# Kernel optimization log

Measured on AMD Instinct MI355X. Metric: run time of the kernel, lower is better.

The kernel has to match this reference:

```python
import jax, jax.numpy as jnp
import numpy as np

HIDDEN = 512
NUM_HEAD = 8
HEAD_DIM = HIDDEN // NUM_HEAD


def setup_inputs() -> dict:
    key = jax.random.key(0)
    ks = jax.random.split(key, 12)
    B, S = 8, 1024
    inp = {
        "v": jax.random.normal(ks[0], (B, S, HIDDEN), dtype=jnp.float32),
        "k": jax.random.normal(ks[1], (B, S, HIDDEN), dtype=jnp.float32),
        "q": jax.random.normal(ks[2], (B, S, HIDDEN), dtype=jnp.float32),
        "mask": jnp.zeros((B, 1, 1, S), dtype=bool),
    }
    scale = 1.0 / np.sqrt(HIDDEN)
    inp["Wv"] = jax.random.normal(ks[3], (HIDDEN, HIDDEN), dtype=jnp.float32) * scale
    inp["bv"] = jax.random.normal(ks[4], (HIDDEN,), dtype=jnp.float32) * scale
    inp["Wk"] = jax.random.normal(ks[5], (HIDDEN, HIDDEN), dtype=jnp.float32) * scale
    inp["bk"] = jax.random.normal(ks[6], (HIDDEN,), dtype=jnp.float32) * scale
    inp["Wq"] = jax.random.normal(ks[7], (HIDDEN, HIDDEN), dtype=jnp.float32) * scale
    inp["bq"] = jax.random.normal(ks[8], (HIDDEN,), dtype=jnp.float32) * scale
    inp["Wm"] = jax.random.normal(ks[9], (HIDDEN, HIDDEN), dtype=jnp.float32) * scale
    inp["bm"] = jax.random.normal(ks[10], (HIDDEN,), dtype=jnp.float32) * scale
    return inp


def _split_heads(x):
    # [B, S, H*D] -> [B, H, S, D]
    B, S, _ = x.shape
    return x.reshape(B, S, NUM_HEAD, HEAD_DIM).transpose(0, 2, 1, 3)


def reference(v, k, q, mask, Wv, bv, Wk, bk, Wq, bq, Wm, bm):
    B, S, _ = q.shape
    # linear projections (torch Linear: x @ W.T + b)
    vh = _split_heads(v @ Wv.T + bv)
    kh = _split_heads(k @ Wk.T + bk)
    qh = _split_heads(q @ Wq.T + bq)
    scale = 1.0 / jnp.sqrt(jnp.asarray(HEAD_DIM, dtype=qh.dtype))
    scores = jnp.einsum('bhqd,bhkd->bhqk', qh, kh) * scale
    scores = jnp.where(mask, jnp.asarray(-10000.0, dtype=scores.dtype), scores)
    att_map = jax.nn.softmax(scores, axis=-1)
    atted = jnp.einsum('bhqk,bhkd->bhqd', att_map, vh)
    atted = atted.transpose(0, 2, 1, 3).reshape(B, S, HIDDEN)
    atted = atted @ Wm.T + bm
    return atted, att_map
```

## Files before the change

### kernel.cpp

```cpp
#include <hip/hip_runtime.h>
#include <cstddef>

#define SEQ 1024
#define HID 512
#define NH 8
#define HD 64

typedef __attribute__((ext_vector_type(8))) short bf16x8;
typedef __attribute__((ext_vector_type(4))) float f32x4;

__device__ inline unsigned short f2bf(float f) {
  unsigned u = __builtin_bit_cast(unsigned, f);
  return (unsigned short)((u + 0x7fffu + ((u >> 16) & 1u)) >> 16);
}

__global__ __launch_bounds__(256) void proj_qkv(
    const float* __restrict__ x0, const float* __restrict__ x1, const float* __restrict__ x2,
    const float* __restrict__ w0, const float* __restrict__ w1, const float* __restrict__ w2,
    const float* __restrict__ b0, const float* __restrict__ b1, const float* __restrict__ b2,
    unsigned short* __restrict__ o0, unsigned short* __restrict__ o1,
    unsigned short* __restrict__ o2) {
  __shared__ short As[128 * 64];
  __shared__ short Bs[128 * 64];

  const int z = blockIdx.z;
  const float* X = z == 0 ? x0 : (z == 1 ? x1 : x2);
  const float* W = z == 0 ? w0 : (z == 1 ? w1 : w2);
  const float* bias = z == 0 ? b0 : (z == 1 ? b1 : b2);
  unsigned short* out = z == 0 ? o0 : (z == 1 ? o1 : o2);
  const float scale = z == 0 ? 0.125f : 1.0f;

  const int t = threadIdx.x;
  const int lane = t & 63, wid = t >> 6;
  const int lg = lane >> 4, lr = lane & 15;
  const int wm = (wid >> 1) * 64, wn = (wid & 1) * 64;
  const int m0 = blockIdx.y * 128, n0 = blockIdx.x * 128;

  f32x4 acc[4][4];
  const f32x4 zf = {0.f, 0.f, 0.f, 0.f};
#pragma unroll
  for (int mg = 0; mg < 4; ++mg)
#pragma unroll
    for (int ng = 0; ng < 4; ++ng) acc[mg][ng] = zf;

  for (int k0 = 0; k0 < 512; k0 += 64) {
    __syncthreads();
#pragma unroll
    for (int i = 0; i < 4; ++i) {
      const int gi = t + i * 256;
      const int r = gi >> 3, g = gi & 7;
      const int dst = r * 64 + ((g ^ (r & 7)) * 8);
      {
        const float* src = X + (size_t)(m0 + r) * 512 + k0 + g * 8;
        const float4 a = *reinterpret_cast<const float4*>(src);
        const float4 b2 = *reinterpret_cast<const float4*>(src + 4);
        union { bf16x8 v; unsigned short u[8]; } p;
        p.u[0] = f2bf(a.x);  p.u[1] = f2bf(a.y);  p.u[2] = f2bf(a.z);  p.u[3] = f2bf(a.w);
        p.u[4] = f2bf(b2.x); p.u[5] = f2bf(b2.y); p.u[6] = f2bf(b2.z); p.u[7] = f2bf(b2.w);
        *reinterpret_cast<bf16x8*>(As + dst) = p.v;
      }
      {
        const float* srcw = W + (size_t)(n0 + r) * 512 + k0 + g * 8;
        const float4 wa = *reinterpret_cast<const float4*>(srcw);
        const float4 wb = *reinterpret_cast<const float4*>(srcw + 4);
        union { bf16x8 v; unsigned short u[8]; } q;
        q.u[0] = f2bf(wa.x); q.u[1] = f2bf(wa.y); q.u[2] = f2bf(wa.z); q.u[3] = f2bf(wa.w);
        q.u[4] = f2bf(wb.x); q.u[5] = f2bf(wb.y); q.u[6] = f2bf(wb.z); q.u[7] = f2bf(wb.w);
        *reinterpret_cast<bf16x8*>(Bs + dst) = q.v;
      }
    }
    __syncthreads();

#pragma unroll
    for (int c = 0; c < 2; ++c) {
      bf16x8 af[4], bfr[4];
#pragma unroll
      for (int mg = 0; mg < 4; ++mg) {
        const int r = wm + mg * 16 + lr;
        af[mg] = *reinterpret_cast<const bf16x8*>(As + r * 64 + (((lg + 4 * c) ^ (r & 7)) * 8));
      }
#pragma unroll
      for (int ng = 0; ng < 4; ++ng) {
        const int r = wn + ng * 16 + lr;
        bfr[ng] = *reinterpret_cast<const bf16x8*>(Bs + r * 64 + (((lg + 4 * c) ^ (r & 7)) * 8));
      }
#pragma unroll
      for (int mg = 0; mg < 4; ++mg)
#pragma unroll
        for (int ng = 0; ng < 4; ++ng)
          acc[mg][ng] =
              __builtin_amdgcn_mfma_f32_16x16x32_bf16(af[mg], bfr[ng], acc[mg][ng], 0, 0, 0);
    }
  }

  float bv[4];
#pragma unroll
  for (int ng = 0; ng < 4; ++ng) bv[ng] = bias[n0 + wn + ng * 16 + lr];

#pragma unroll
  for (int mg = 0; mg < 4; ++mg) {
#pragma unroll
    for (int reg = 0; reg < 4; ++reg) {
      const int m = m0 + wm + mg * 16 + 4 * lg + reg;
#pragma unroll
      for (int ng = 0; ng < 4; ++ng) {
        const int n = n0 + wn + ng * 16 + lr;
        const float cval = (acc[mg][ng][reg] + bv[ng]) * scale;
        const int b = m >> 10, s = m & 1023, h = n >> 6, d = n & 63;
        if (z == 2)
          out[(((size_t)(b * NH + h)) * HD + d) * SEQ + s] = f2bf(cval);
        else
          out[(((size_t)(b * NH + h)) * SEQ + s) * HD + d] = f2bf(cval);
      }
    }
  }
}

__global__ __launch_bounds__(256) void proj_out(const unsigned short* __restrict__ Xb,
                                                const float* __restrict__ W,
                                                const float* __restrict__ bias,
                                                float* __restrict__ outv) {
  __shared__ short As[128 * 64];
  __shared__ short Bs[128 * 64];

  const int t = threadIdx.x;
  const int lane = t & 63, wid = t >> 6;
  const int lg = lane >> 4, lr = lane & 15;
  const int wm = (wid >> 1) * 64, wn = (wid & 1) * 64;
  const int m0 = blockIdx.y * 128, n0 = blockIdx.x * 128;

  f32x4 acc[4][4];
  const f32x4 zf = {0.f, 0.f, 0.f, 0.f};
#pragma unroll
  for (int mg = 0; mg < 4; ++mg)
#pragma unroll
    for (int ng = 0; ng < 4; ++ng) acc[mg][ng] = zf;

  for (int k0 = 0; k0 < 512; k0 += 64) {
    __syncthreads();
#pragma unroll
    for (int i = 0; i < 4; ++i) {
      const int gi = t + i * 256;
      const int r = gi >> 3, g = gi & 7;
      const int dst = r * 64 + ((g ^ (r & 7)) * 8);
      *reinterpret_cast<bf16x8*>(As + dst) =
          *reinterpret_cast<const bf16x8*>(Xb + (size_t)(m0 + r) * 512 + k0 + g * 8);
      const float* srcw = W + (size_t)(n0 + r) * 512 + k0 + g * 8;
      const float4 wa = *reinterpret_cast<const float4*>(srcw);
      const float4 wb = *reinterpret_cast<const float4*>(srcw + 4);
      union { bf16x8 v; unsigned short u[8]; } q;
      q.u[0] = f2bf(wa.x); q.u[1] = f2bf(wa.y); q.u[2] = f2bf(wa.z); q.u[3] = f2bf(wa.w);
      q.u[4] = f2bf(wb.x); q.u[5] = f2bf(wb.y); q.u[6] = f2bf(wb.z); q.u[7] = f2bf(wb.w);
      *reinterpret_cast<bf16x8*>(Bs + dst) = q.v;
    }
    __syncthreads();

#pragma unroll
    for (int c = 0; c < 2; ++c) {
      bf16x8 af[4], bfr[4];
#pragma unroll
      for (int mg = 0; mg < 4; ++mg) {
        const int r = wm + mg * 16 + lr;
        af[mg] = *reinterpret_cast<const bf16x8*>(As + r * 64 + (((lg + 4 * c) ^ (r & 7)) * 8));
      }
#pragma unroll
      for (int ng = 0; ng < 4; ++ng) {
        const int r = wn + ng * 16 + lr;
        bfr[ng] = *reinterpret_cast<const bf16x8*>(Bs + r * 64 + (((lg + 4 * c) ^ (r & 7)) * 8));
      }
#pragma unroll
      for (int mg = 0; mg < 4; ++mg)
#pragma unroll
        for (int ng = 0; ng < 4; ++ng)
          acc[mg][ng] =
              __builtin_amdgcn_mfma_f32_16x16x32_bf16(af[mg], bfr[ng], acc[mg][ng], 0, 0, 0);
    }
  }

  float bv[4];
#pragma unroll
  for (int ng = 0; ng < 4; ++ng) bv[ng] = bias[n0 + wn + ng * 16 + lr];

#pragma unroll
  for (int mg = 0; mg < 4; ++mg) {
#pragma unroll
    for (int reg = 0; reg < 4; ++reg) {
      const int m = m0 + wm + mg * 16 + 4 * lg + reg;
#pragma unroll
      for (int ng = 0; ng < 4; ++ng) {
        const int n = n0 + wn + ng * 16 + lr;
        __builtin_nontemporal_store(acc[mg][ng][reg] + bv[ng], outv + (size_t)m * 512 + n);
      }
    }
  }
}

__global__ __launch_bounds__(256, 4) void attn_fused(const unsigned short* __restrict__ qh,
                                                     const unsigned short* __restrict__ kh,
                                                     const unsigned short* __restrict__ vhT,
                                                     const unsigned char* __restrict__ mask,
                                                     float* __restrict__ att_map,
                                                     unsigned short* __restrict__ atted) {
  __shared__ short Vt[64 * 128];
  __shared__ short Pw4[4][2048];
  __shared__ float maskf[1024];

  const int t = threadIdx.x;
  const int lane = t & 63, wid = t >> 6;
  const int lg = lane >> 4, lr = lane & 15;
  const int qt = blockIdx.x & 15;
  const int bh = blockIdx.x >> 4;
  const int b = bh >> 3, h = bh & 7;
  const int q0 = qt * 64 + wid * 16;

  const unsigned short* Qb = qh + ((size_t)bh * SEQ + q0) * HD;
  const unsigned short* Kb = kh + (size_t)bh * SEQ * HD;
  const unsigned short* Vb = vhT + (size_t)bh * HD * SEQ;
  const unsigned char* mrow = mask + (size_t)b * SEQ;

#pragma unroll
  for (int i = 0; i < 4; ++i) {
    const int idx = t + i * 256;
    maskf[idx] = mrow[idx] ? -10000.f : 0.f;
  }

  bf16x8 qf[2];
#pragma unroll
  for (int c = 0; c < 2; ++c)
    qf[c] = *reinterpret_cast<const bf16x8*>(Qb + (size_t)lr * HD + lg * 8 + 32 * c);

  const f32x4 zf = {0.f, 0.f, 0.f, 0.f};
  f32x4 oacc[4] = {zf, zf, zf, zf};
  float rs = 0.f;
  short* Pw = Pw4[wid];

  for (int kt = 0; kt < 8; ++kt) {
    __syncthreads();
#pragma unroll
    for (int i = 0; i < 4; ++i) {
      const int gi = t + i * 256;
      const int d = gi >> 4, g = gi & 15;
      const int slot = (g & 8) | ((g & 7) ^ (d & 7));
      *reinterpret_cast<bf16x8*>(Vt + d * 128 + slot * 8) =
          *reinterpret_cast<const bf16x8*>(Vb + (size_t)d * SEQ + kt * 128 + g * 8);
    }
    __syncthreads();

#pragma unroll
    for (int cg = 0; cg < 8; ++cg) {
      const int r = kt * 128 + cg * 16 + lr;
      f32x4 s = zf;
#pragma unroll
      for (int c = 0; c < 2; ++c) {
        const bf16x8 kf =
            *reinterpret_cast<const bf16x8*>(Kb + (size_t)r * HD + (lg + 4 * c) * 8);
        s = __builtin_amdgcn_mfma_f32_16x16x32_bf16(kf, qf[c], s, 0, 0, 0);
      }
      const float4 madd =
          *reinterpret_cast<const float4*>(maskf + kt * 128 + cg * 16 + 4 * lg);
      const float p0 = __expf(s[0] + madd.x);
      const float p1 = __expf(s[1] + madd.y);
      const float p2 = __expf(s[2] + madd.z);
      const float p3 = __expf(s[3] + madd.w);
      rs += (p0 + p1) + (p2 + p3);
      uint2 pr;
      pr.x = (unsigned)f2bf(p0) | ((unsigned)f2bf(p1) << 16);
      pr.y = (unsigned)f2bf(p2) | ((unsigned)f2bf(p3) << 16);
      const int gk = 2 * cg + (lg >> 1);
      *reinterpret_cast<uint2*>(Pw + lr * 128 + ((gk ^ (lr & 7)) * 8) + (lg & 1) * 4) = pr;
    }

#pragma unroll
    for (int c = 0; c < 4; ++c) {
      const bf16x8 pa =
          *reinterpret_cast<const bf16x8*>(Pw + lr * 128 + (((lg + 4 * c) ^ (lr & 7)) * 8));
#pragma unroll
      for (int ng = 0; ng < 4; ++ng) {
        const int d = ng * 16 + lr;
        const int gidx = 4 * c + lg;
        const int slot = (gidx & 8) | ((gidx & 7) ^ (d & 7));
        const bf16x8 vf = *reinterpret_cast<const bf16x8*>(Vt + d * 128 + slot * 8);
        oacc[ng] = __builtin_amdgcn_mfma_f32_16x16x32_bf16(pa, vf, oacc[ng], 0, 0, 0);
      }
    }
  }

  rs += __shfl_xor(rs, 16);
  rs += __shfl_xor(rs, 32);
  const float inv = 1.f / rs;

  {
    float invq[4];
#pragma unroll
    for (int reg = 0; reg < 4; ++reg) invq[reg] = __shfl(inv, 4 * lg + reg);
#pragma unroll
    for (int ng = 0; ng < 4; ++ng) {
#pragma unroll
      for (int reg = 0; reg < 4; ++reg) {
        const int q = q0 + 4 * lg + reg;
        const int d = ng * 16 + lr;
        atted[((size_t)b * SEQ + q) * HID + h * HD + d] = f2bf(oacc[ng][reg] * invq[reg]);
      }
    }
  }

  float* arow = att_map + ((size_t)bh * SEQ + q0 + lr) * SEQ + 4 * lg;

  bf16x8 kfA[4][2], kfB[4][2];
  auto LD = [&](bf16x8 (&kf)[4][2], int it) {
    const int kt = it >> 1, h4 = (it & 1) * 4;
#pragma unroll
    for (int j = 0; j < 4; ++j) {
      const int r = kt * 128 + (h4 + j) * 16 + lr;
#pragma unroll
      for (int c = 0; c < 2; ++c)
        kf[j][c] =
            *reinterpret_cast<const bf16x8*>(Kb + (size_t)r * HD + (lg + 4 * c) * 8);
    }
  };
  auto CS = [&](bf16x8 (&kf)[4][2], int it) {
    const int kt = it >> 1, h4 = (it & 1) * 4;
#pragma unroll
    for (int j = 0; j < 4; ++j) {
      f32x4 s = zf;
      s = __builtin_amdgcn_mfma_f32_16x16x32_bf16(kf[j][0], qf[0], s, 0, 0, 0);
      s = __builtin_amdgcn_mfma_f32_16x16x32_bf16(kf[j][1], qf[1], s, 0, 0, 0);
      const int kbase = kt * 128 + (h4 + j) * 16;
      const float4 madd = *reinterpret_cast<const float4*>(maskf + kbase + 4 * lg);
      f32x4 w;
      w.x = __expf(s[0] + madd.x) * inv;
      w.y = __expf(s[1] + madd.y) * inv;
      w.z = __expf(s[2] + madd.z) * inv;
      w.w = __expf(s[3] + madd.w) * inv;
      __builtin_nontemporal_store(w, reinterpret_cast<f32x4*>(arow + kbase));
    }
  };

  LD(kfA, 0);
#pragma unroll
  for (int ip = 0; ip < 8; ++ip) {
    LD(kfB, ip * 2 + 1);
    CS(kfA, ip * 2);
    if (ip * 2 + 2 < 16) LD(kfA, ip * 2 + 2);
    CS(kfB, ip * 2 + 1);
  }
}

extern "C" void kernel_launch(void* const* d_in, const int* in_sizes, int n_in,
                              void* d_out, int out_size, void* d_ws, size_t ws_size,
                              hipStream_t stream) {
  const float* v = (const float*)d_in[0];
  const float* k = (const float*)d_in[1];
  const float* q = (const float*)d_in[2];
  const unsigned char* mask = (const unsigned char*)d_in[3];
  const float* Wv = (const float*)d_in[4];
  const float* bv = (const float*)d_in[5];
  const float* Wk = (const float*)d_in[6];
  const float* bk = (const float*)d_in[7];
  const float* Wq = (const float*)d_in[8];
  const float* bq = (const float*)d_in[9];
  const float* Wm = (const float*)d_in[10];
  const float* bm = (const float*)d_in[11];

  float* out_atted = (float*)d_out;
  float* out_att = out_atted + (size_t)8 * SEQ * HID;

  const size_t TN = (size_t)8 * SEQ * HID;
  unsigned short* qh = (unsigned short*)d_ws;
  unsigned short* kh = qh + TN;
  unsigned short* vhT = kh + TN;
  unsigned short* aw = vhT + TN;

  proj_qkv<<<dim3(4, 64, 3), 256, 0, stream>>>(q, k, v, Wq, Wk, Wv, bq, bk, bv, qh, kh, vhT);

  attn_fused<<<dim3(1024), 256, 0, stream>>>(qh, kh, vhT, mask, out_att, aw);

  proj_out<<<dim3(4, 64), 256, 0, stream>>>(aw, Wm, bm, out_atted);
}
```

Measured before the change: 210.7 us.

## Stage att_map writes through LDS for coalesced rows and remap block order

The second pass of the attention kernel now writes normalized probabilities into a swizzled per-wave LDS tile, then reads them back so each row is stored as contiguous 512-byte segments instead of scattered 16-byte column chunks. Shared memory is unioned into one buffer so the staging tile reuses the V and P space. The block index is also remapped so eight consecutive blocks cover different heads of the same query tile. The intent is better coalescing of the large fp32 att_map write, at the cost of extra LDS traffic and losing nontemporal stores.

```diff
diff --git a/kernel.cpp b/kernel.cpp
--- a/kernel.cpp
+++ b/kernel.cpp
@@ -201,15 +201,18 @@
                                                      const unsigned char* __restrict__ mask,
                                                      float* __restrict__ att_map,
                                                      unsigned short* __restrict__ atted) {
-  __shared__ short Vt[64 * 128];
-  __shared__ short Pw4[4][2048];
-  __shared__ float maskf[1024];
+  __shared__ __align__(16) char smem[36864];
+  short* Vt = (short*)smem;
+  float* maskf = (float*)(smem + 32768);
 
   const int t = threadIdx.x;
   const int lane = t & 63, wid = t >> 6;
   const int lg = lane >> 4, lr = lane & 15;
-  const int qt = blockIdx.x & 15;
-  const int bh = blockIdx.x >> 4;
+  const int i = blockIdx.x;
+  const int c8 = i & 7;
+  const int j = i >> 3;
+  const int bh = ((j >> 4) << 3) | c8;
+  const int qt = j & 15;
   const int b = bh >> 3, h = bh & 7;
   const int q0 = qt * 64 + wid * 16;
 
@@ -219,8 +222,8 @@
   const unsigned char* mrow = mask + (size_t)b * SEQ;
 
 #pragma unroll
-  for (int i = 0; i < 4; ++i) {
-    const int idx = t + i * 256;
+  for (int ii = 0; ii < 4; ++ii) {
+    const int idx = t + ii * 256;
     maskf[idx] = mrow[idx] ? -10000.f : 0.f;
   }
 
@@ -232,13 +235,13 @@
   const f32x4 zf = {0.f, 0.f, 0.f, 0.f};
   f32x4 oacc[4] = {zf, zf, zf, zf};
   float rs = 0.f;
-  short* Pw = Pw4[wid];
+  short* Pw = (short*)(smem + 16384) + wid * 2048;
 
   for (int kt = 0; kt < 8; ++kt) {
     __syncthreads();
 #pragma unroll
-    for (int i = 0; i < 4; ++i) {
-      const int gi = t + i * 256;
+    for (int ii = 0; ii < 4; ++ii) {
+      const int gi = t + ii * 256;
       const int d = gi >> 4, g = gi & 15;
       const int slot = (g & 8) | ((g & 7) ^ (d & 7));
       *reinterpret_cast<bf16x8*>(Vt + d * 128 + slot * 8) =
@@ -304,45 +307,59 @@
     }
   }
 
-  float* arow = att_map + ((size_t)bh * SEQ + q0 + lr) * SEQ + 4 * lg;
+  __syncthreads();
+
+  float* Sf = (float*)(smem + wid * 8192);
+  float* arow_base = att_map + ((size_t)bh * SEQ + q0) * SEQ;
 
   bf16x8 kfA[4][2], kfB[4][2];
-  auto LD = [&](bf16x8 (&kf)[4][2], int it) {
-    const int kt = it >> 1, h4 = (it & 1) * 4;
-#pragma unroll
-    for (int j = 0; j < 4; ++j) {
-      const int r = kt * 128 + (h4 + j) * 16 + lr;
+  auto LD = [&](bf16x8 (&kf)[4][2], int ih) {
+    const int kt = ih >> 1, h4 = (ih & 1) * 4;
+#pragma unroll
+    for (int jj = 0; jj < 4; ++jj) {
+      const int r = kt * 128 + (h4 + jj) * 16 + lr;
 #pragma unroll
       for (int c = 0; c < 2; ++c)
-        kf[j][c] =
+        kf[jj][c] =
             *reinterpret_cast<const bf16x8*>(Kb + (size_t)r * HD + (lg + 4 * c) * 8);
     }
   };
-  auto CS = [&](bf16x8 (&kf)[4][2], int it) {
-    const int kt = it >> 1, h4 = (it & 1) * 4;
-#pragma unroll
-    for (int j = 0; j < 4; ++j) {
+  auto CS = [&](bf16x8 (&kf)[4][2], int ih) {
+    const int kt = ih >> 1, h4 = (ih & 1) * 4;
+#pragma unroll
+    for (int jj = 0; jj < 4; ++jj) {
+      const int cg = h4 + jj;
       f32x4 s = zf;
-      s = __builtin_amdgcn_mfma_f32_16x16x32_bf16(kf[j][0], qf[0], s, 0, 0, 0);
-      s = __builtin_amdgcn_mfma_f32_16x16x32_bf16(kf[j][1], qf[1], s, 0, 0, 0);
-      const int kbase = kt * 128 + (h4 + j) * 16;
-      const float4 madd = *reinterpret_cast<const float4*>(maskf + kbase + 4 * lg);
+      s = __builtin_amdgcn_mfma_f32_16x16x32_bf16(kf[jj][0], qf[0], s, 0, 0, 0);
+      s = __builtin_amdgcn_mfma_f32_16x16x32_bf16(kf[jj][1], qf[1], s, 0, 0, 0);
+      const float4 madd =
+          *reinterpret_cast<const float4*>(maskf + kt * 128 + cg * 16 + 4 * lg);
       f32x4 w;
       w.x = __expf(s[0] + madd.x) * inv;
       w.y = __expf(s[1] + madd.y) * inv;
       w.z = __expf(s[2] + madd.z) * inv;
       w.w = __expf(s[3] + madd.w) * inv;
-      __builtin_nontemporal_store(w, reinterpret_cast<f32x4*>(arow + kbase));
+      const int g = cg * 4 + lg;
+      *reinterpret_cast<f32x4*>(Sf + lr * 128 + ((g ^ (lr & 7)) * 4)) = w;
     }
   };
 
+  const int r2l = lane >> 5;
+  const int gcol = lane & 31;
+
   LD(kfA, 0);
-#pragma unroll
-  for (int ip = 0; ip < 8; ++ip) {
-    LD(kfB, ip * 2 + 1);
-    CS(kfA, ip * 2);
-    if (ip * 2 + 2 < 16) LD(kfA, ip * 2 + 2);
-    CS(kfB, ip * 2 + 1);
+  for (int kt = 0; kt < 8; ++kt) {
+    LD(kfB, 2 * kt + 1);
+    CS(kfA, 2 * kt);
+    if (kt < 7) LD(kfA, 2 * kt + 2);
+    CS(kfB, 2 * kt + 1);
+#pragma unroll
+    for (int it2 = 0; it2 < 8; ++it2) {
+      const int r2 = it2 * 2 + r2l;
+      const f32x4 w4 =
+          *reinterpret_cast<const f32x4*>(Sf + r2 * 128 + ((gcol ^ (r2 & 7)) * 4));
+      *reinterpret_cast<f32x4*>(arow_base + (size_t)r2 * SEQ + kt * 128 + gcol * 4) = w4;
+    }
   }
 }
 
```

Result: slower. 216.2 us (+2.6%).
